# Kernel optimization log

Measured on AMD Instinct MI355X. Metric: run time of the kernel, lower is better.

## Reference

```python
import jax, jax.numpy as jnp
import numpy as np

LATENT_DIM = 128
NUM_QUANTIZERS = 8
CODEBOOK_SIZE = 1024


def setup_inputs() -> dict:
    key = jax.random.key(0)
    k1, k2 = jax.random.split(key)
    z = jax.random.normal(k1, (8, LATENT_DIM, 4096), dtype=jnp.float32)
    scale = 1.0 / np.sqrt(LATENT_DIM)
    codebooks = jax.random.uniform(
        k2, (NUM_QUANTIZERS, CODEBOOK_SIZE, LATENT_DIM),
        minval=-scale, maxval=scale, dtype=jnp.float32)
    return {"z": z, "codebooks": codebooks}


def _nearest_indices(x_flat, codebook):
    # x_flat: [N, D], codebook: [K, D] -> [N] argmin of squared L2 distance
    d = (jnp.sum(x_flat * x_flat, axis=1, keepdims=True)
         - 2.0 * x_flat @ codebook.T
         + jnp.sum(codebook * codebook, axis=1)[None, :])
    return jnp.argmin(d, axis=1)


def reference(z, codebooks):
    # z: [B, D, S] -> z_bsd: [B, S, D]
    z_bsd = jnp.transpose(z, (0, 2, 1))
    B, S, D = z_bsd.shape
    Q, K, _ = codebooks.shape

    residual = z_bsd
    quantized = jnp.zeros_like(z_bsd)
    idx_list = []
    for q in range(Q):  # small fixed loop over quantizer stages
        cb = codebooks[q]
        idx = _nearest_indices(residual.reshape(-1, D), cb).reshape(B, S)
        selected = cb[idx]                       # [B, S, D] gather
        quantized = quantized + selected
        residual = residual - jax.lax.stop_gradient(selected)
        idx_list.append(idx)
    indices = jnp.stack(idx_list, axis=-1)        # [B, S, Q]

    commitment_loss = jnp.mean(
        (z_bsd - jax.lax.stop_gradient(quantized)) ** 2)
    quantized_st = z_bsd + jax.lax.stop_gradient(quantized - z_bsd)

    def _perplexity(ix):  # ix: [B, S] codes for one quantizer
        counts = jnp.zeros((K,), jnp.float32).at[ix.reshape(-1)].add(1.0)
        probs = counts / jnp.maximum(counts.sum(), 1.0)
        entropy = -jnp.sum(probs * jnp.log(probs + 1e-10))
        return jnp.exp(entropy)

    perplexity = jnp.mean(jax.vmap(_perplexity, in_axes=2)(indices))

    return (jnp.transpose(quantized_st, (0, 2, 1)),  # [B, D, S]
            indices, commitment_loss, perplexity)
```

## Files before the change

kernel.cpp:

```cpp
#include <hip/hip_runtime.h>
#include <math.h>
#include <stdint.h>

#define D       128
#define KCODES  1024
#define NQ      8
#define BATCH   8
#define SLEN    4096
#define NPTS    (BATCH*SLEN)
#define TM      64

typedef __attribute__((address_space(1))) const void GV;
typedef __attribute__((address_space(3))) void LV;
__device__ __forceinline__ void gload16(const void* g, void* l) {
    __builtin_amdgcn_global_load_lds((GV*)g, (LV*)l, 16, 0, 0);
}

__global__ void k_zero(int* hist, double* csum) {
    int t = blockIdx.x * blockDim.x + threadIdx.x;
    if (t < NQ * KCODES) hist[t] = 0;
    if (t == 0) *csum = 0.0;
}

__global__ void k_c2(const float* __restrict__ cbs, float* __restrict__ c2f) {
    int i = blockIdx.x * blockDim.x + threadIdx.x;
    const float* row = cbs + (size_t)i * D;
    float r8[8];
    #pragma unroll
    for (int j = 0; j < 8; ++j) r8[j] = __fmul_rn(row[j], row[j]);
    for (int d = 8; d < 128; d += 8)
        #pragma unroll
        for (int j = 0; j < 8; ++j)
            r8[j] = __fadd_rn(r8[j], __fmul_rn(row[d + j], row[d + j]));
    float s01 = __fadd_rn(r8[0], r8[1]);
    float s23 = __fadd_rn(r8[2], r8[3]);
    float s45 = __fadd_rn(r8[4], r8[5]);
    float s67 = __fadd_rn(r8[6], r8[7]);
    c2f[i] = __fadd_rn(__fadd_rn(s01, s23), __fadd_rn(s45, s67));
}

__global__ __launch_bounds__(256) void k_init(const float* __restrict__ z,
                                              float* __restrict__ resid,
                                              float* __restrict__ quant) {
    __shared__ float xt[64][129];
    int b = blockIdx.x >> 6, st = blockIdx.x & 63;
    int s0 = st * 64;
    for (int it = 0; it < 32; ++it) {
        int flat = it * 256 + threadIdx.x;
        int d = flat >> 6, sl = flat & 63;
        xt[sl][d] = z[((size_t)(b * D + d)) * SLEN + s0 + sl];
    }
    __syncthreads();
    for (int it = 0; it < 8; ++it) {
        int flat = it * 256 + threadIdx.x;
        int sl = flat >> 5, dq = (flat & 31) * 4;
        size_t o = (size_t)(b * SLEN + s0 + sl) * D + dq;
        float4 r;
        r.x = xt[sl][dq]; r.y = xt[sl][dq + 1];
        r.z = xt[sl][dq + 2]; r.w = xt[sl][dq + 3];
        *(float4*)(resid + o) = r;
        float4 zz; zz.x = zz.y = zz.z = zz.w = 0.0f;
        *(float4*)(quant + o) = zz;
    }
}

__global__ __launch_bounds__(256, 2) void k_argmin(const float* __restrict__ cb,
                                                   const float* __restrict__ c2,
                                                   const float* __restrict__ resid,
                                                   float* __restrict__ pbest,
                                                   int* __restrict__ pidx) {
    __shared__ __align__(16) float xs[TM][132];
    __shared__ __align__(16) float cs[4][2][256];
    __shared__ __align__(16) float ccl[4][128];
    __shared__ float redS[4][TM];
    __shared__ int   redI[4][TM];

    int tid = threadIdx.x;
    int u = blockIdx.x;
    int pblk = u >> 1, half = u & 1;
    int pbase = pblk * TM;
    int l = tid & 63, w = tid >> 6;
    int pl = l & 7, cl = l >> 3;

    const char* cwb = (const char*)cb + ((size_t)(half * 512 + w * 128) << 9);
    char* csw = (char*)&cs[w][0][0];
    const char* xsb = (const char*)&xs[0][0];

#define ISSUE(T) { \
    const char* _src = cwb + (((T) >> 5) << 15) + ((size_t)l << 9) + (((T) & 31) << 4); \
    gload16(_src, csw + (((T) & 1) << 10)); }

    ISSUE(0);
    if (l < 32) {
        float4 cv = *(const float4*)(c2 + half * 512 + w * 128 + l * 4);
        *(float4*)&ccl[w][l * 4] = cv;
    }

    #pragma unroll
    for (int it = 0; it < 8; ++it) {
        int e = (it * 256 + tid) * 4;
        int p = e >> 7, d = e & 127;
        *(float4*)&xs[p][d] = *(const float4*)(resid + (size_t)(pbase + p) * D + d);
    }
    __syncthreads();

    if (tid < TM) {
        float r8[8];
        #pragma unroll
        for (int j = 0; j < 8; ++j) r8[j] = __fmul_rn(xs[tid][j], xs[tid][j]);
        for (int i = 8; i < 128; i += 8)
            #pragma unroll
            for (int j = 0; j < 8; ++j)
                r8[j] = __fadd_rn(r8[j], __fmul_rn(xs[tid][i + j], xs[tid][i + j]));
        float s01 = __fadd_rn(r8[0], r8[1]);
        float s23 = __fadd_rn(r8[2], r8[3]);
        float s45 = __fadd_rn(r8[4], r8[5]);
        float s67 = __fadd_rn(r8[6], r8[7]);
        xs[tid][128] = __fadd_rn(__fadd_rn(s01, s23), __fadd_rn(s45, s67));
    }
    __syncthreads();

    float xxr[8];
    #pragma unroll
    for (int i = 0; i < 8; ++i) xxr[i] = xs[pl + 8 * i][128];

    float acc[8][8];
    #pragma unroll
    for (int i = 0; i < 8; ++i)
        #pragma unroll
        for (int j = 0; j < 8; ++j) acc[i][j] = 0.0f;
    float best[8]; int bidx[8];
    #pragma unroll
    for (int i = 0; i < 8; ++i) { best[i] = 3.4e38f; bidx[i] = 0; }

    #pragma unroll 1
    for (int t = 0; t < 64; ++t) {
        if (t < 63) {
            ISSUE(t + 1);
            asm volatile("s_waitcnt vmcnt(1)" ::: "memory");
        } else {
            asm volatile("s_waitcnt vmcnt(0)" ::: "memory");
        }
        const char* cbuf = csw + ((t & 1) << 10) + (cl << 4);
        const char* xrow = xsb + pl * 528 + ((t & 31) << 4);
        float4 xf[8];
        #pragma unroll
        for (int i = 0; i < 8; ++i)
            xf[i] = *(const float4*)(xrow + i * 4224);
        #pragma unroll
        for (int jp = 0; jp < 4; ++jp) {
            float4 cf0 = *(const float4*)(cbuf + ((2 * jp)     << 7));
            float4 cf1 = *(const float4*)(cbuf + ((2 * jp + 1) << 7));
            #pragma unroll
            for (int i = 0; i < 8; ++i) {
                acc[i][2*jp]   = __fmaf_rn(xf[i].x, cf0.x, acc[i][2*jp]);
                acc[i][2*jp]   = __fmaf_rn(xf[i].y, cf0.y, acc[i][2*jp]);
                acc[i][2*jp]   = __fmaf_rn(xf[i].z, cf0.z, acc[i][2*jp]);
                acc[i][2*jp]   = __fmaf_rn(xf[i].w, cf0.w, acc[i][2*jp]);
                acc[i][2*jp+1] = __fmaf_rn(xf[i].x, cf1.x, acc[i][2*jp+1]);
                acc[i][2*jp+1] = __fmaf_rn(xf[i].y, cf1.y, acc[i][2*jp+1]);
                acc[i][2*jp+1] = __fmaf_rn(xf[i].z, cf1.z, acc[i][2*jp+1]);
                acc[i][2*jp+1] = __fmaf_rn(xf[i].w, cf1.w, acc[i][2*jp+1]);
            }
        }
        if ((t & 31) == 31) {
            int c = t >> 5;
            #pragma unroll
            for (int j = 0; j < 8; ++j) {
                float cc = ccl[w][(c << 6) + cl + (j << 3)];
                int k = half * 512 + (w << 7) + (c << 6) + cl + (j << 3);
                #pragma unroll
                for (int i = 0; i < 8; ++i) {
                    float t1  = __fadd_rn(xxr[i], __fmul_rn(-2.0f, acc[i][j]));
                    float dsc = __fadd_rn(t1, cc);
                    if (dsc < best[i]) { best[i] = dsc; bidx[i] = k; }
                    acc[i][j] = 0.0f;
                }
            }
        }
    }

    #pragma unroll
    for (int i = 0; i < 8; ++i) {
        float b = best[i]; int bi = bidx[i];
        #pragma unroll
        for (int off = 8; off < 64; off <<= 1) {
            float b2 = __shfl_xor(b, off, 64);
            int  bi2 = __shfl_xor(bi, off, 64);
            if (b2 < b || (b2 == b && bi2 < bi)) { b = b2; bi = bi2; }
        }
        if (cl == 0) { redS[w][pl + 8 * i] = b; redI[w][pl + 8 * i] = bi; }
    }
    __syncthreads();
    if (tid < TM) {
        float b = redS[0][tid]; int bi = redI[0][tid];
        #pragma unroll
        for (int ww = 1; ww < 4; ++ww) {
            float b2 = redS[ww][tid]; int bi2 = redI[ww][tid];
            if (b2 < b || (b2 == b && bi2 < bi)) { b = b2; bi = bi2; }
        }
        pbest[half * NPTS + pbase + tid] = b;
        pidx [half * NPTS + pbase + tid] = bi;
    }
#undef ISSUE
}

__global__ void k_update(const float* __restrict__ cb,
                         const float* __restrict__ pbest,
                         const int* __restrict__ pidx,
                         int* __restrict__ idx,
                         float* __restrict__ resid, float* __restrict__ quant) {
    int gid = blockIdx.x * blockDim.x + threadIdx.x;
    int n = gid >> 5, d4 = (gid & 31) * 4;
    float a = pbest[n], b = pbest[NPTS + n];
    int ia = pidx[n], ib = pidx[NPTS + n];
    int k = (b < a) ? ib : ia;
    if ((gid & 31) == 0) idx[n] = k;
    float4 c = *(const float4*)(cb + (size_t)k * D + d4);
    size_t o = (size_t)n * D + d4;
    float4 r = *(const float4*)(resid + o);
    float4 q = *(const float4*)(quant + o);
    r.x = __fsub_rn(r.x, c.x); r.y = __fsub_rn(r.y, c.y);
    r.z = __fsub_rn(r.z, c.z); r.w = __fsub_rn(r.w, c.w);
    q.x = __fadd_rn(q.x, c.x); q.y = __fadd_rn(q.y, c.y);
    q.z = __fadd_rn(q.z, c.z); q.w = __fadd_rn(q.w, c.w);
    *(float4*)(resid + o) = r;
    *(float4*)(quant + o) = q;
}

__global__ __launch_bounds__(256) void k_out0(const float* __restrict__ z,
                                              const float* __restrict__ quant,
                                              float* __restrict__ out0,
                                              double* __restrict__ csum) {
    __shared__ float xt[64][129];
    __shared__ double wsum[4];
    int b = blockIdx.x >> 6, st = blockIdx.x & 63;
    int s0 = st * 64;
    for (int it = 0; it < 8; ++it) {
        int flat = it * 256 + threadIdx.x;
        int sl = flat >> 5, dq = (flat & 31) * 4;
        float4 q = *(const float4*)(quant + (size_t)(b * SLEN + s0 + sl) * D + dq);
        xt[sl][dq] = q.x; xt[sl][dq + 1] = q.y;
        xt[sl][dq + 2] = q.z; xt[sl][dq + 3] = q.w;
    }
    __syncthreads();
    double v = 0.0;
    for (int it = 0; it < 32; ++it) {
        int flat = it * 256 + threadIdx.x;
        int d = flat >> 6, sl = flat & 63;
        size_t o = ((size_t)(b * D + d)) * SLEN + s0 + sl;
        float zz = z[o], qq = xt[sl][d];
        out0[o] = __fadd_rn(zz, __fsub_rn(qq, zz));
        float e = __fsub_rn(zz, qq);
        v += (double)e * (double)e;
    }
    for (int off = 32; off > 0; off >>= 1) v += __shfl_down(v, off, 64);
    int lane = threadIdx.x & 63, wv = threadIdx.x >> 6;
    if (lane == 0) wsum[wv] = v;
    __syncthreads();
    if (threadIdx.x == 0) {
        double tsum = wsum[0] + wsum[1] + wsum[2] + wsum[3];
        atomicAdd(csum, tsum);
    }
}

__global__ void k_outidx(const int* __restrict__ idx, float* __restrict__ out1) {
    int o = blockIdx.x * blockDim.x + threadIdx.x;
    int q = o & 7, n = o >> 3;
    out1[o] = (float)idx[q * NPTS + n];
}

__global__ void k_hist(const int* __restrict__ idx, int* __restrict__ hist) {
    int o = blockIdx.x * blockDim.x + threadIdx.x;
    int q = o >> 15;
    atomicAdd(&hist[q * KCODES + idx[o]], 1);
}

__global__ __launch_bounds__(256) void k_final(const int* __restrict__ hist,
                                               const double* __restrict__ csum,
                                               float* __restrict__ outs) {
    __shared__ double sh[256];
    double perp = 0.0;
    for (int q = 0; q < NQ; ++q) {
        double h = 0.0;
        for (int k = threadIdx.x; k < KCODES; k += 256) {
            double p = (double)hist[q * KCODES + k] / (double)NPTS;
            h -= p * log(p + 1e-10);
        }
        sh[threadIdx.x] = h; __syncthreads();
        for (int off = 128; off > 0; off >>= 1) {
            if (threadIdx.x < off) sh[threadIdx.x] += sh[threadIdx.x + off];
            __syncthreads();
        }
        if (threadIdx.x == 0) perp += exp(sh[0]);
        __syncthreads();
    }
    if (threadIdx.x == 0) {
        outs[0] = (float)(*csum / (double)((size_t)NPTS * D));
        outs[1] = (float)(perp / (double)NQ);
    }
}

extern "C" void kernel_launch(void* const* d_in, const int* in_sizes, int n_in,
                              void* d_out, int out_size, void* d_ws, size_t ws_size,
                              hipStream_t stream) {
    const float* z  = (const float*)d_in[0];
    const float* cb = (const float*)d_in[1];
    float* out0 = (float*)d_out;
    float* out1 = out0 + 4194304;
    float* outs = out1 + 262144;

    char* w = (char*)d_ws;
    float* resid  = (float*)w;
    float* quant  = (float*)(w + 16777216);
    int*   idx    = (int*)(w + 33554432);
    int*   hist   = (int*)(w + 34603008);
    double* csum  = (double*)(w + 34635776);
    float* c2f    = (float*)(w + 34635840);
    float* pbest  = (float*)(w + 34668608);
    int*   pidx   = (int*)(w + 34930752);

    k_zero<<<32, 256, 0, stream>>>(hist, csum);
    k_c2<<<32, 256, 0, stream>>>(cb, c2f);
    k_init<<<512, 256, 0, stream>>>(z, resid, quant);

    for (int q = 0; q < NQ; ++q) {
        const float* cbq = cb + (size_t)q * KCODES * D;
        k_argmin<<<2 * NPTS / TM, 256, 0, stream>>>(cbq, c2f + q * KCODES, resid,
                                                    pbest, pidx);
        k_update<<<NPTS * 32 / 256, 256, 0, stream>>>(cbq, pbest, pidx,
                                                      idx + q * NPTS, resid, quant);
    }

    k_out0<<<512, 256, 0, stream>>>(z, quant, out0, csum);
    k_outidx<<<NPTS * NQ / 256, 256, 0, stream>>>(idx, out1);
    k_hist<<<NPTS * NQ / 256, 256, 0, stream>>>(idx, hist);
    k_final<<<1, 256, 0, stream>>>(hist, csum, outs);
}
```

Before: 1.167 ms.

## Deepen codebook LDS prefetch to four buffers and process two k-slices per iteration

Codebook staging via global_load_lds grows from double to quad buffering, so two 16-byte slices are issued ahead and the wait allows two loads in flight. The inner loop now handles two slices per iteration with a restructured register schedule that loads codebook vectors per half and re-reads x rows inside the i loop. The launch-bounds occupancy hint of 2 is dropped. This aims to hide global latency and cut loop and wait overhead, at the cost of more LDS and possibly more VGPR pressure or extra LDS reads of x.

Result: slower. 1.220 ms (+4.5%).

```diff
diff --git a/kernel.cpp b/kernel.cpp
--- a/kernel.cpp
+++ b/kernel.cpp
@@ -64,13 +64,13 @@
     }
 }
 
-__global__ __launch_bounds__(256, 2) void k_argmin(const float* __restrict__ cb,
-                                                   const float* __restrict__ c2,
-                                                   const float* __restrict__ resid,
-                                                   float* __restrict__ pbest,
-                                                   int* __restrict__ pidx) {
+__global__ __launch_bounds__(256) void k_argmin(const float* __restrict__ cb,
+                                                const float* __restrict__ c2,
+                                                const float* __restrict__ resid,
+                                                float* __restrict__ pbest,
+                                                int* __restrict__ pidx) {
     __shared__ __align__(16) float xs[TM][132];
-    __shared__ __align__(16) float cs[4][2][256];
+    __shared__ __align__(16) float cs[4][4][256];
     __shared__ __align__(16) float ccl[4][128];
     __shared__ float redS[4][TM];
     __shared__ int   redI[4][TM];
@@ -88,9 +88,10 @@
 
 #define ISSUE(T) { \
     const char* _src = cwb + (((T) >> 5) << 15) + ((size_t)l << 9) + (((T) & 31) << 4); \
-    gload16(_src, csw + (((T) & 1) << 10)); }
+    gload16(_src, csw + (((T) & 3) << 10)); }
 
     ISSUE(0);
+    ISSUE(1);
     if (l < 32) {
         float4 cv = *(const float4*)(c2 + half * 512 + w * 128 + l * 4);
         *(float4*)&ccl[w][l * 4] = cv;
@@ -134,37 +135,49 @@
     for (int i = 0; i < 8; ++i) { best[i] = 3.4e38f; bidx[i] = 0; }
 
     #pragma unroll 1
-    for (int t = 0; t < 64; ++t) {
-        if (t < 63) {
-            ISSUE(t + 1);
-            asm volatile("s_waitcnt vmcnt(1)" ::: "memory");
+    for (int P = 0; P < 32; ++P) {
+        if (P < 31) {
+            ISSUE(2 * P + 2);
+            ISSUE(2 * P + 3);
+            asm volatile("s_waitcnt vmcnt(2)" ::: "memory");
         } else {
             asm volatile("s_waitcnt vmcnt(0)" ::: "memory");
         }
-        const char* cbuf = csw + ((t & 1) << 10) + (cl << 4);
-        const char* xrow = xsb + pl * 528 + ((t & 31) << 4);
-        float4 xf[8];
-        #pragma unroll
-        for (int i = 0; i < 8; ++i)
-            xf[i] = *(const float4*)(xrow + i * 4224);
-        #pragma unroll
-        for (int jp = 0; jp < 4; ++jp) {
-            float4 cf0 = *(const float4*)(cbuf + ((2 * jp)     << 7));
-            float4 cf1 = *(const float4*)(cbuf + ((2 * jp + 1) << 7));
+        int gA = 2 * P;
+        const char* cbufA = csw + ((gA & 3) << 10) + (cl << 4);
+        const char* cbufB = csw + (((gA + 1) & 3) << 10) + (cl << 4);
+        const char* xrowA = xsb + pl * 528 + ((gA & 31) << 4);
+        const char* xrowB = xrowA + 16;
+        #pragma unroll
+        for (int jh = 0; jh < 2; ++jh) {
+            float4 cA[4], cB[4];
+            #pragma unroll
+            for (int jc = 0; jc < 4; ++jc) {
+                cA[jc] = *(const float4*)(cbufA + ((jh * 4 + jc) << 7));
+                cB[jc] = *(const float4*)(cbufB + ((jh * 4 + jc) << 7));
+            }
             #pragma unroll
             for (int i = 0; i < 8; ++i) {
-                acc[i][2*jp]   = __fmaf_rn(xf[i].x, cf0.x, acc[i][2*jp]);
-                acc[i][2*jp]   = __fmaf_rn(xf[i].y, cf0.y, acc[i][2*jp]);
-                acc[i][2*jp]   = __fmaf_rn(xf[i].z, cf0.z, acc[i][2*jp]);
-                acc[i][2*jp]   = __fmaf_rn(xf[i].w, cf0.w, acc[i][2*jp]);
-                acc[i][2*jp+1] = __fmaf_rn(xf[i].x, cf1.x, acc[i][2*jp+1]);
-                acc[i][2*jp+1] = __fmaf_rn(xf[i].y, cf1.y, acc[i][2*jp+1]);
-                acc[i][2*jp+1] = __fmaf_rn(xf[i].z, cf1.z, acc[i][2*jp+1]);
-                acc[i][2*jp+1] = __fmaf_rn(xf[i].w, cf1.w, acc[i][2*jp+1]);
+                float4 xA = *(const float4*)(xrowA + i * 4224);
+                float4 xB = *(const float4*)(xrowB + i * 4224);
+                #pragma unroll
+                for (int jc = 0; jc < 4; ++jc) {
+                    int jj = jh * 4 + jc;
+                    float a = acc[i][jj];
+                    a = __fmaf_rn(xA.x, cA[jc].x, a);
+                    a = __fmaf_rn(xA.y, cA[jc].y, a);
+                    a = __fmaf_rn(xA.z, cA[jc].z, a);
+                    a = __fmaf_rn(xA.w, cA[jc].w, a);
+                    a = __fmaf_rn(xB.x, cB[jc].x, a);
+                    a = __fmaf_rn(xB.y, cB[jc].y, a);
+                    a = __fmaf_rn(xB.z, cB[jc].z, a);
+                    a = __fmaf_rn(xB.w, cB[jc].w, a);
+                    acc[i][jj] = a;
+                }
             }
         }
-        if ((t & 31) == 31) {
-            int c = t >> 5;
+        if ((P & 15) == 15) {
+            int c = P >> 4;
             #pragma unroll
             for (int j = 0; j < 8; ++j) {
                 float cc = ccl[w][(c << 6) + cl + (j << 3)];
```
